# Optimization experiments

Measured on AMD Instinct MI355X. Metric: run time of the kernel, lower is better.

The kernel has to match this reference:

```python
import jax, jax.numpy as jnp
import numpy as np

N_NODES = 20000
N_EDGES = 320000
NODE_DIM = 512
HIDDEN = 512
N_GRAPHS = 64


def setup_inputs() -> dict:
    key = jax.random.key(0)
    ks = jax.random.split(key, 12)
    s = 0.02
    return {
        "joint_x": jax.random.normal(ks[0], (N_NODES, NODE_DIM), jnp.float32),
        "joint_edge_index": jax.random.randint(ks[1], (2, N_EDGES), 0, N_NODES, dtype=jnp.int32),
        "joint_batch": jnp.sort(jax.random.randint(ks[2], (N_NODES,), 0, N_GRAPHS, dtype=jnp.int32)),
        "W_g1": jax.random.normal(ks[3], (NODE_DIM, HIDDEN), jnp.float32) * s,
        "b_g1": jnp.zeros((HIDDEN,), jnp.float32),
        "W_g2": jax.random.normal(ks[4], (HIDDEN, HIDDEN), jnp.float32) * s,
        "b_g2": jnp.zeros((HIDDEN,), jnp.float32),
        "W_c1": jax.random.normal(ks[5], (HIDDEN, HIDDEN // 2), jnp.float32) * s,
        "b_c1": jnp.zeros((HIDDEN // 2,), jnp.float32),
        "W_c2": jax.random.normal(ks[6], (HIDDEN // 2, 1), jnp.float32) * s,
        "b_c2": jnp.zeros((1,), jnp.float32),
    }


def _gin_layer(h, src, dst, W, b):
    # GINConv(nn=Linear, eps=0): nn((1+eps)*x_i + sum_{j->i} x_j)
    agg = jax.ops.segment_sum(h[src], dst, num_segments=N_NODES)  # [N, D]
    return (h + agg) @ W + b


def reference(joint_x, joint_edge_index, joint_batch, W_g1, b_g1, W_g2, b_g2, W_c1, b_c1, W_c2, b_c2):
    src, dst = joint_edge_index[0], joint_edge_index[1]
    h = _gin_layer(joint_x, src, dst, W_g1, b_g1)  # [N, HIDDEN]
    h = _gin_layer(h, src, dst, W_g2, b_g2)        # [N, HIDDEN]
    pooled = jax.ops.segment_sum(h, joint_batch, num_segments=N_GRAPHS)  # [G, HIDDEN]
    z = jax.nn.relu(pooled @ W_c1 + b_c1)
    score = z @ W_c2 + b_c2                        # [G, 1]
    return jax.nn.sigmoid(score).squeeze(-1)       # [G]
```

## Files before the change

### kernel.cpp

```cpp
#include <hip/hip_runtime.h>
#include <math.h>

constexpr int N_NODES = 20000;
constexpr int DIM = 512;
constexpr int NG = 64;
constexpr int CAP = 64;
constexpr int KCH = 80;
constexpr int NCHUNK = (N_NODES + KCH - 1) / KCH;
constexpr int NSPLIT = 2;
constexpr int RSPLIT = 10;
constexpr int CPS = (NCHUNK + RSPLIT - 1) / RSPLIT;
constexpr int CGS = 32;
constexpr int CSTR = 16;
constexpr int NODE_BLOCKS = (N_NODES + 3) / 4;
constexpr int INIT_BLOCKS = (N_NODES + 255) / 256;
constexpr int GEMM_TILES = 17 * 4;
constexpr int KSPLIT_TILES = GEMM_TILES * 2;
constexpr int PQ_ELEMS = 513 * 256;
constexpr int EPT = 2;
constexpr int EDGE_BLOCKS = (320000 + 256 * EPT - 1) / (256 * EPT);

__device__ __forceinline__ int lower_bound_i(const int* __restrict__ a, int n, int v) {
  int lo = 0, hi = n;
  while (lo < hi) {
    int mid = (lo + hi) >> 1;
    if (a[mid] < v) lo = mid + 1; else hi = mid;
  }
  return lo;
}

__global__ __launch_bounds__(256) void node_init(const int* __restrict__ batch,
                                                 int* __restrict__ cursor,
                                                 float* __restrict__ ng,
                                                 float* __restrict__ cgpad, int n_nodes) {
  int node = blockIdx.x * 256 + threadIdx.x;
  if (node < n_nodes) cursor[(size_t)node * CSTR] = 0;
  if (blockIdx.x == 0 && threadIdx.x < 64) {
    int gg = threadIdx.x;
    int s0 = lower_bound_i(batch, n_nodes, gg);
    int e0 = lower_bound_i(batch, n_nodes, gg + 1);
    ng[gg] = (float)(e0 - s0);
    cgpad[gg * CGS] = 0.f;
  }
}

__device__ void gemm_stack_tile(const float* __restrict__ A0, const float* __restrict__ extra,
                                const float* __restrict__ B, const float* __restrict__ B2,
                                float* __restrict__ C,
                                int N, int K, int R0, int tile, int kbeg, int kend,
                                float* As, float* Bs, int tid) {
  int bm = (tile >> 2) * 32;
  int bn = (tile & 3) * 64;
  int tx = tid & 15;
  int ty = tid >> 4;
  int ar = tid >> 3;
  int ac = (tid & 7) * 2;
  int br = tid >> 4;
  int bc = (tid & 15) * 4;
  float acc[2][4] = {};
  for (int k0 = kbeg; k0 < kend; k0 += 16) {
    int row = bm + ar;
    float2 av = make_float2(0.f, 0.f);
    if (row < R0)       av = *(const float2*)(A0 + (size_t)row * K + k0 + ac);
    else if (row == R0) av = *(const float2*)(extra + k0 + ac);
    As[(ac + 0) * 34 + ar] = av.x;
    As[(ac + 1) * 34 + ar] = av.y;
    size_t boff = (size_t)(k0 + br) * N + bn + bc;
    float4 bv = *(const float4*)(B + boff);
    if (B2) {
      float4 b2 = *(const float4*)(B2 + boff);
      bv.x += b2.x; bv.y += b2.y; bv.z += b2.z; bv.w += b2.w;
    }
    *(float4*)&Bs[br * 68 + bc] = bv;
    __syncthreads();
#pragma unroll
    for (int kk = 0; kk < 16; ++kk) {
      float2 a01 = *(const float2*)&As[kk * 34 + ty * 2];
      float4 b4  = *(const float4*)&Bs[kk * 68 + tx * 4];
      acc[0][0] = fmaf(a01.x, b4.x, acc[0][0]); acc[0][1] = fmaf(a01.x, b4.y, acc[0][1]);
      acc[0][2] = fmaf(a01.x, b4.z, acc[0][2]); acc[0][3] = fmaf(a01.x, b4.w, acc[0][3]);
      acc[1][0] = fmaf(a01.y, b4.x, acc[1][0]); acc[1][1] = fmaf(a01.y, b4.y, acc[1][1]);
      acc[1][2] = fmaf(a01.y, b4.z, acc[1][2]); acc[1][3] = fmaf(a01.y, b4.w, acc[1][3]);
    }
    __syncthreads();
  }
#pragma unroll
  for (int i = 0; i < 2; ++i) {
    int m = bm + ty * 2 + i;
    if (m > R0) continue;
    *(float4*)&C[(size_t)m * N + bn + tx * 4] =
        make_float4(acc[i][0], acc[i][1], acc[i][2], acc[i][3]);
  }
}

__global__ __launch_bounds__(256) void fill_and_Q(const int* __restrict__ srcI,
                                                  const int* __restrict__ dstI,
                                                  const int* __restrict__ batch,
                                                  int* __restrict__ cursor,
                                                  int* __restrict__ edst,
                                                  float* __restrict__ cgpad,
                                                  const float* __restrict__ Wg2,
                                                  const float* __restrict__ bg2,
                                                  const float* __restrict__ Wc1,
                                                  float* __restrict__ Q, int n_edges) {
  __shared__ float As[16 * 34];
  __shared__ float Bs[16 * 68];
  __shared__ int hist[64];
  int b = blockIdx.x;
  int t = threadIdx.x;
  if (b < KSPLIT_TILES) {
    int ks = b & 1;
    int tile = b >> 1;
    gemm_stack_tile(Wg2, bg2, Wc1, nullptr, Q + (size_t)ks * PQ_ELEMS,
                    256, 512, 512, tile, ks * 256, ks * 256 + 256, As, Bs, t);
  } else {
    int eb = b - KSPLIT_TILES;
    if (t < 64) hist[t] = 0;
    __syncthreads();
    int base = eb * (256 * EPT) + t;
    int s[EPT], d[EPT], c[EPT];
    bool v[EPT];
#pragma unroll
    for (int u = 0; u < EPT; ++u) {
      int i = base + u * 256;
      v[u] = i < n_edges;
      s[u] = v[u] ? srcI[i] : 0;
    }
#pragma unroll
    for (int u = 0; u < EPT; ++u) {
      int i = base + u * 256;
      d[u] = v[u] ? dstI[i] : 0;
    }
#pragma unroll
    for (int u = 0; u < EPT; ++u)
      if (v[u]) c[u] = atomicAdd(&cursor[(size_t)s[u] * CSTR], 1);
#pragma unroll
    for (int u = 0; u < EPT; ++u)
      if (v[u]) edst[(size_t)s[u] * CAP + c[u]] = d[u];
#pragma unroll
    for (int u = 0; u < EPT; ++u)
      if (v[u]) atomicAdd(&hist[batch[d[u]]], 1);
    __syncthreads();
    if (t < 64 && hist[t] != 0) atomicAdd(&cgpad[t * CGS], (float)hist[t]);
  }
}

__global__ __launch_bounds__(256) void wT_and_P(const int* __restrict__ batch,
                                                const int* __restrict__ deg,
                                                const int* __restrict__ edst,
                                                float* __restrict__ wT,
                                                const float* __restrict__ Wg1,
                                                const float* __restrict__ bg1,
                                                const float* __restrict__ Q,
                                                float* __restrict__ P, int n_nodes) {
  __shared__ float As[16 * 34];
  __shared__ float Bs[16 * 68];
  int b = blockIdx.x;
  int t = threadIdx.x;
  if (b < KSPLIT_TILES) {
    int ks = b & 1;
    int tile = b >> 1;
    gemm_stack_tile(Wg1, bg1, Q, Q + PQ_ELEMS, P + (size_t)ks * PQ_ELEMS,
                    256, 512, 512, tile, ks * 256, ks * 256 + 256, As, Bs, t);
  } else {
    int node = (b - KSPLIT_TILES) * 4 + (t >> 6);
    int g = t & 63;
    if (node >= n_nodes) return;
    int end = deg[(size_t)node * CSTR];
    const int* nb = edst + (size_t)node * CAP;
    float acc = (batch[node] == g) ? 1.f : 0.f;
    int i = 0;
    for (; i + 7 < end; i += 8) {
      int d0 = nb[i], d1 = nb[i + 1], d2 = nb[i + 2], d3 = nb[i + 3];
      int d4 = nb[i + 4], d5 = nb[i + 5], d6 = nb[i + 6], d7 = nb[i + 7];
      int b0 = batch[d0], b1 = batch[d1], b2 = batch[d2], b3 = batch[d3];
      int b4 = batch[d4], b5 = batch[d5], b6 = batch[d6], b7 = batch[d7];
      acc += ((float)(b0 == g) + (float)(b1 == g)) + ((float)(b2 == g) + (float)(b3 == g)) +
             ((float)(b4 == g) + (float)(b5 == g)) + ((float)(b6 == g) + (float)(b7 == g));
    }
    for (; i < end; ++i) acc += (float)(batch[nb[i]] == g);
    wT[(size_t)node * 64 + g] = acc;
  }
}

#define LOADX(X, KB)                                                      \
  _Pragma("unroll")                                                       \
  for (int t_ = 0; t_ < 4; ++t_) {                                        \
    X[t_][0] = x2[(size_t)(k0 + (KB) + t_) * 256 + ncol];                 \
    X[t_][1] = x2[(size_t)(k0 + (KB) + t_) * 256 + ncol + 64];            \
  }

#define COMPX(X, KB)                                                      \
  _Pragma("unroll")                                                       \
  for (int t_ = 0; t_ < 4; ++t_) {                                        \
    const float4* cp_ = (const float4*)&scT[(KB) + t_][w * 8];            \
    float4 cA_ = cp_[0], cB_ = cp_[1];                                    \
    float cv_[8] = {cA_.x, cA_.y, cA_.z, cA_.w, cB_.x, cB_.y, cB_.z, cB_.w}; \
    _Pragma("unroll")                                                     \
    for (int q_ = 0; q_ < 8; ++q_) {                                      \
      acc[q_][0].x = fmaf(cv_[q_], X[t_][0].x, acc[q_][0].x);             \
      acc[q_][0].y = fmaf(cv_[q_], X[t_][0].y, acc[q_][0].y);             \
      acc[q_][1].x = fmaf(cv_[q_], X[t_][1].x, acc[q_][1].x);             \
      acc[q_][1].y = fmaf(cv_[q_], X[t_][1].y, acc[q_][1].y);             \
    }                                                                     \
  }

__global__ __launch_bounds__(512, 4) void ct_ugemm(const float* __restrict__ wT,
                                                   const int* __restrict__ deg,
                                                   const int* __restrict__ edst,
                                                   const float* __restrict__ x,
                                                   float* __restrict__ Upart, int n_nodes) {
  __shared__ float scT[KCH][64];
  int c = blockIdx.y;
  int nx = blockIdx.x;
  int t = threadIdx.x;
  int w = t >> 6;
  int g = t & 63;
  int k0 = c * KCH;
  int kmax = (n_nodes - k0) < KCH ? (n_nodes - k0) : KCH;
  for (int i = w; i < kmax; i += 8) {
    int node = k0 + i;
    float acc1 = wT[(size_t)node * 64 + g];
    int end = deg[(size_t)node * CSTR];
    const int* nb = edst + (size_t)node * CAP;
    int j = 0;
    for (; j + 7 < end; j += 8) {
      int d0 = nb[j], d1 = nb[j + 1], d2 = nb[j + 2], d3 = nb[j + 3];
      int d4 = nb[j + 4], d5 = nb[j + 5], d6 = nb[j + 6], d7 = nb[j + 7];
      float v0 = wT[(size_t)d0 * 64 + g], v1 = wT[(size_t)d1 * 64 + g];
      float v2 = wT[(size_t)d2 * 64 + g], v3 = wT[(size_t)d3 * 64 + g];
      float v4 = wT[(size_t)d4 * 64 + g], v5 = wT[(size_t)d5 * 64 + g];
      float v6 = wT[(size_t)d6 * 64 + g], v7 = wT[(size_t)d7 * 64 + g];
      acc1 += ((v0 + v1) + (v2 + v3)) + ((v4 + v5) + (v6 + v7));
    }
    for (; j + 3 < end; j += 4) {
      int d0 = nb[j], d1 = nb[j + 1], d2 = nb[j + 2], d3 = nb[j + 3];
      acc1 += wT[(size_t)d0 * 64 + g] + wT[(size_t)d1 * 64 + g] +
              wT[(size_t)d2 * 64 + g] + wT[(size_t)d3 * 64 + g];
    }
    for (; j < end; ++j) acc1 += wT[(size_t)nb[j] * 64 + g];
    scT[i][g] = acc1;
  }
  __syncthreads();
  const float2* x2 = (const float2*)x;
  int ncol = nx * 128 + g;
  float2 acc[8][2];
#pragma unroll
  for (int q = 0; q < 8; ++q) {
    acc[q][0] = make_float2(0.f, 0.f);
    acc[q][1] = make_float2(0.f, 0.f);
  }
  float2 xa[4][2], xb[4][2];
  LOADX(xa, 0);
  for (int kk = 0; kk < kmax; kk += 8) {
    LOADX(xb, kk + 4);
    COMPX(xa, kk);
    if (kk + 8 < kmax) { LOADX(xa, kk + 8); }
    COMPX(xb, kk + 4);
  }
  float2* up = (float2*)Upart;
#pragma unroll
  for (int q = 0; q < 8; ++q) {
    int gg = w * 8 + q;
    up[((size_t)c * 64 + gg) * 256 + ncol] = acc[q][0];
    up[((size_t)c * 64 + gg) * 256 + ncol + 64] = acc[q][1];
  }
}

__global__ __launch_bounds__(128) void reduce_U(const float* __restrict__ Upart,
                                                float* __restrict__ Ured) {
  int g = blockIdx.x;
  int s = blockIdx.y;
  int t = threadIdx.x;
  int c0 = s * CPS;
  int c1 = (c0 + CPS < NCHUNK) ? c0 + CPS : NCHUNK;
  const float4* up = (const float4*)Upart;
  float4 acc = make_float4(0.f, 0.f, 0.f, 0.f);
  for (int c = c0; c < c1; ++c) {
    float4 v = up[((size_t)c * 64 + g) * 128 + t];
    acc.x += v.x; acc.y += v.y; acc.z += v.z; acc.w += v.w;
  }
  ((float4*)Ured)[((size_t)s * 64 + g) * 128 + t] = acc;
}

__global__ __launch_bounds__(256) void head(const float* __restrict__ Ured,
                                            const float* __restrict__ P,
                                            const float* __restrict__ Q,
                                            const float* __restrict__ ng,
                                            const float* __restrict__ cgpad,
                                            const float* __restrict__ bc1,
                                            const float* __restrict__ Wc2,
                                            const float* __restrict__ bc2,
                                            float* __restrict__ out) {
  int g = blockIdx.x;
  int j = threadIdx.x;
  const float* Wc0 = P;
  const float* Wc1p = P + (size_t)PQ_ELEMS;
  const float* v1a = P + (size_t)512 * 256;
  const float* v1b = P + (size_t)PQ_ELEMS + (size_t)512 * 256;
  const float* v2a = Q + (size_t)512 * 256;
  const float* v2b = Q + (size_t)PQ_ELEMS + (size_t)512 * 256;
  __shared__ float p[512];
  float s0 = 0.f, s1 = 0.f;
#pragma unroll
  for (int s = 0; s < RSPLIT; ++s) {
    s0 += Ured[((size_t)s * 64 + g) * DIM + j];
    s1 += Ured[((size_t)s * 64 + g) * DIM + 256 + j];
  }
  p[j] = s0;
  p[j + 256] = s1;
  __syncthreads();
  float cg = ng[g] + cgpad[g * CGS];
  float acc = bc1[j] + cg * (v1a[j] + v1b[j]) + ng[g] * (v2a[j] + v2b[j]);
  for (int k = 0; k < 512; ++k) {
    float w = Wc0[k * 256 + j] + Wc1p[k * 256 + j];
    acc = fmaf(p[k], w, acc);
  }
  float z = fmaxf(acc, 0.f);
  float part = z * Wc2[j];
  for (int off = 32; off > 0; off >>= 1) part += __shfl_down(part, off, 64);
  __shared__ float red[4];
  if ((j & 63) == 0) red[j >> 6] = part;
  __syncthreads();
  if (j == 0) {
    float tot = red[0] + red[1] + red[2] + red[3] + bc2[0];
    out[g] = 1.f / (1.f + expf(-tot));
  }
}

extern "C" void kernel_launch(void* const* d_in, const int* in_sizes, int n_in,
                              void* d_out, int out_size, void* d_ws, size_t ws_size,
                              hipStream_t stream) {
  const float* x    = (const float*)d_in[0];
  const int*   ei   = (const int*)d_in[1];
  const int*   batch= (const int*)d_in[2];
  const float* Wg1  = (const float*)d_in[3];
  const float* bg1  = (const float*)d_in[4];
  const float* Wg2  = (const float*)d_in[5];
  const float* bg2  = (const float*)d_in[6];
  const float* Wc1  = (const float*)d_in[7];
  const float* bc1  = (const float*)d_in[8];
  const float* Wc2  = (const float*)d_in[9];
  const float* bc2  = (const float*)d_in[10];
  float* out = (float*)d_out;

  int n_edges = in_sizes[1] / 2;
  int n_nodes = in_sizes[2];
  const int* srcI = ei;
  const int* dstI = ei + n_edges;

  char* ws = (char*)d_ws;
  size_t off = 0;
  auto alloc = [&](size_t bytes) { char* p = ws + off; off += (bytes + 255) & ~(size_t)255; return p; };
  float* wT    = (float*)alloc((size_t)N_NODES * 64 * sizeof(float));
  float* Upart = (float*)alloc((size_t)NCHUNK * 64 * DIM * sizeof(float));
  float* Ured  = (float*)alloc((size_t)RSPLIT * 64 * DIM * sizeof(float));
  float* Q     = (float*)alloc((size_t)2 * PQ_ELEMS * sizeof(float));
  float* P     = (float*)alloc((size_t)2 * PQ_ELEMS * sizeof(float));
  float* ng    = (float*)alloc(NG * sizeof(float));
  float* cgpad = (float*)alloc(NG * CGS * sizeof(float));
  int* cursor  = (int*)alloc((size_t)N_NODES * CSTR * sizeof(int));
  int* edst    = (int*)alloc((size_t)N_NODES * CAP * sizeof(int));

  node_init<<<INIT_BLOCKS, 256, 0, stream>>>(batch, cursor, ng, cgpad, n_nodes);
  fill_and_Q<<<KSPLIT_TILES + EDGE_BLOCKS, 256, 0, stream>>>(srcI, dstI, batch, cursor, edst,
                                                             cgpad, Wg2, bg2, Wc1, Q, n_edges);
  wT_and_P<<<KSPLIT_TILES + NODE_BLOCKS, 256, 0, stream>>>(batch, cursor, edst, wT,
                                                           Wg1, bg1, Q, P, n_nodes);
  ct_ugemm<<<dim3(NSPLIT, NCHUNK), 512, 0, stream>>>(wT, cursor, edst, x, Upart, n_nodes);
  reduce_U<<<dim3(64, RSPLIT), 128, 0, stream>>>(Upart, Ured);
  head<<<NG, 256, 0, stream>>>(Ured, P, Q, ng, cgpad, bc1, Wc2, bc2, out);
}
```

Measured before the change: 234.7 us.

## Split wT build into own kernel and precompute cT before the GEMM

Result: faster. 223.2 us (-4.9%).

```diff
diff --git a/kernel.cpp b/kernel.cpp
--- a/kernel.cpp
+++ b/kernel.cpp
@@ -145,10 +145,33 @@
   }
 }
 
-__global__ __launch_bounds__(256) void wT_and_P(const int* __restrict__ batch,
+__global__ __launch_bounds__(256) void build_wT(const int* __restrict__ batch,
                                                 const int* __restrict__ deg,
                                                 const int* __restrict__ edst,
-                                                float* __restrict__ wT,
+                                                float* __restrict__ wT, int n_nodes) {
+  int node = blockIdx.x * 4 + (threadIdx.x >> 6);
+  int g = threadIdx.x & 63;
+  if (node >= n_nodes) return;
+  int end = deg[(size_t)node * CSTR];
+  const int* nb = edst + (size_t)node * CAP;
+  float acc = (batch[node] == g) ? 1.f : 0.f;
+  int i = 0;
+  for (; i + 7 < end; i += 8) {
+    int d0 = nb[i], d1 = nb[i + 1], d2 = nb[i + 2], d3 = nb[i + 3];
+    int d4 = nb[i + 4], d5 = nb[i + 5], d6 = nb[i + 6], d7 = nb[i + 7];
+    int b0 = batch[d0], b1 = batch[d1], b2 = batch[d2], b3 = batch[d3];
+    int b4 = batch[d4], b5 = batch[d5], b6 = batch[d6], b7 = batch[d7];
+    acc += ((float)(b0 == g) + (float)(b1 == g)) + ((float)(b2 == g) + (float)(b3 == g)) +
+           ((float)(b4 == g) + (float)(b5 == g)) + ((float)(b6 == g) + (float)(b7 == g));
+  }
+  for (; i < end; ++i) acc += (float)(batch[nb[i]] == g);
+  wT[(size_t)node * 64 + g] = acc;
+}
+
+__global__ __launch_bounds__(256) void cT_and_P(const float* __restrict__ wT,
+                                                const int* __restrict__ deg,
+                                                const int* __restrict__ edst,
+                                                float* __restrict__ cT,
                                                 const float* __restrict__ Wg1,
                                                 const float* __restrict__ bg1,
                                                 const float* __restrict__ Q,
@@ -166,20 +189,26 @@
     int node = (b - KSPLIT_TILES) * 4 + (t >> 6);
     int g = t & 63;
     if (node >= n_nodes) return;
+    float acc = wT[(size_t)node * 64 + g];
     int end = deg[(size_t)node * CSTR];
     const int* nb = edst + (size_t)node * CAP;
-    float acc = (batch[node] == g) ? 1.f : 0.f;
     int i = 0;
     for (; i + 7 < end; i += 8) {
       int d0 = nb[i], d1 = nb[i + 1], d2 = nb[i + 2], d3 = nb[i + 3];
       int d4 = nb[i + 4], d5 = nb[i + 5], d6 = nb[i + 6], d7 = nb[i + 7];
-      int b0 = batch[d0], b1 = batch[d1], b2 = batch[d2], b3 = batch[d3];
-      int b4 = batch[d4], b5 = batch[d5], b6 = batch[d6], b7 = batch[d7];
-      acc += ((float)(b0 == g) + (float)(b1 == g)) + ((float)(b2 == g) + (float)(b3 == g)) +
-             ((float)(b4 == g) + (float)(b5 == g)) + ((float)(b6 == g) + (float)(b7 == g));
-    }
-    for (; i < end; ++i) acc += (float)(batch[nb[i]] == g);
-    wT[(size_t)node * 64 + g] = acc;
+      float v0 = wT[(size_t)d0 * 64 + g], v1 = wT[(size_t)d1 * 64 + g];
+      float v2 = wT[(size_t)d2 * 64 + g], v3 = wT[(size_t)d3 * 64 + g];
+      float v4 = wT[(size_t)d4 * 64 + g], v5 = wT[(size_t)d5 * 64 + g];
+      float v6 = wT[(size_t)d6 * 64 + g], v7 = wT[(size_t)d7 * 64 + g];
+      acc += ((v0 + v1) + (v2 + v3)) + ((v4 + v5) + (v6 + v7));
+    }
+    for (; i + 3 < end; i += 4) {
+      int d0 = nb[i], d1 = nb[i + 1], d2 = nb[i + 2], d3 = nb[i + 3];
+      acc += wT[(size_t)d0 * 64 + g] + wT[(size_t)d1 * 64 + g] +
+             wT[(size_t)d2 * 64 + g] + wT[(size_t)d3 * 64 + g];
+    }
+    for (; i < end; ++i) acc += wT[(size_t)nb[i] * 64 + g];
+    cT[(size_t)node * 64 + g] = acc;
   }
 }
 
@@ -205,11 +234,9 @@
     }                                                                     \
   }
 
-__global__ __launch_bounds__(512, 4) void ct_ugemm(const float* __restrict__ wT,
-                                                   const int* __restrict__ deg,
-                                                   const int* __restrict__ edst,
-                                                   const float* __restrict__ x,
-                                                   float* __restrict__ Upart, int n_nodes) {
+__global__ __launch_bounds__(512, 4) void ugemm(const float* __restrict__ x,
+                                                const float* __restrict__ cT,
+                                                float* __restrict__ Upart, int n_nodes) {
   __shared__ float scT[KCH][64];
   int c = blockIdx.y;
   int nx = blockIdx.x;
@@ -218,28 +245,11 @@
   int g = t & 63;
   int k0 = c * KCH;
   int kmax = (n_nodes - k0) < KCH ? (n_nodes - k0) : KCH;
-  for (int i = w; i < kmax; i += 8) {
-    int node = k0 + i;
-    float acc1 = wT[(size_t)node * 64 + g];
-    int end = deg[(size_t)node * CSTR];
-    const int* nb = edst + (size_t)node * CAP;
-    int j = 0;
-    for (; j + 7 < end; j += 8) {
-      int d0 = nb[j], d1 = nb[j + 1], d2 = nb[j + 2], d3 = nb[j + 3];
-      int d4 = nb[j + 4], d5 = nb[j + 5], d6 = nb[j + 6], d7 = nb[j + 7];
-      float v0 = wT[(size_t)d0 * 64 + g], v1 = wT[(size_t)d1 * 64 + g];
-      float v2 = wT[(size_t)d2 * 64 + g], v3 = wT[(size_t)d3 * 64 + g];
-      float v4 = wT[(size_t)d4 * 64 + g], v5 = wT[(size_t)d5 * 64 + g];
-      float v6 = wT[(size_t)d6 * 64 + g], v7 = wT[(size_t)d7 * 64 + g];
-      acc1 += ((v0 + v1) + (v2 + v3)) + ((v4 + v5) + (v6 + v7));
-    }
-    for (; j + 3 < end; j += 4) {
-      int d0 = nb[j], d1 = nb[j + 1], d2 = nb[j + 2], d3 = nb[j + 3];
-      acc1 += wT[(size_t)d0 * 64 + g] + wT[(size_t)d1 * 64 + g] +
-              wT[(size_t)d2 * 64 + g] + wT[(size_t)d3 * 64 + g];
-    }
-    for (; j < end; ++j) acc1 += wT[(size_t)nb[j] * 64 + g];
-    scT[i][g] = acc1;
+  {
+    const float4* src = (const float4*)(cT + (size_t)k0 * 64);
+    float4* dst = (float4*)(&scT[0][0]);
+    int limit4 = kmax * 16;
+    for (int i = t; i < limit4; i += 512) dst[i] = src[i];
   }
   __syncthreads();
   const float2* x2 = (const float2*)x;
@@ -353,6 +363,7 @@
   size_t off = 0;
   auto alloc = [&](size_t bytes) { char* p = ws + off; off += (bytes + 255) & ~(size_t)255; return p; };
   float* wT    = (float*)alloc((size_t)N_NODES * 64 * sizeof(float));
+  float* cT    = (float*)alloc((size_t)N_NODES * 64 * sizeof(float));
   float* Upart = (float*)alloc((size_t)NCHUNK * 64 * DIM * sizeof(float));
   float* Ured  = (float*)alloc((size_t)RSPLIT * 64 * DIM * sizeof(float));
   float* Q     = (float*)alloc((size_t)2 * PQ_ELEMS * sizeof(float));
@@ -365,9 +376,10 @@
   node_init<<<INIT_BLOCKS, 256, 0, stream>>>(batch, cursor, ng, cgpad, n_nodes);
   fill_and_Q<<<KSPLIT_TILES + EDGE_BLOCKS, 256, 0, stream>>>(srcI, dstI, batch, cursor, edst,
                                                              cgpad, Wg2, bg2, Wc1, Q, n_edges);
-  wT_and_P<<<KSPLIT_TILES + NODE_BLOCKS, 256, 0, stream>>>(batch, cursor, edst, wT,
+  build_wT<<<NODE_BLOCKS, 256, 0, stream>>>(batch, cursor, edst, wT, n_nodes);
+  cT_and_P<<<KSPLIT_TILES + NODE_BLOCKS, 256, 0, stream>>>(wT, cursor, edst, cT,
                                                            Wg1, bg1, Q, P, n_nodes);
-  ct_ugemm<<<dim3(NSPLIT, NCHUNK), 512, 0, stream>>>(wT, cursor, edst, x, Upart, n_nodes);
+  ugemm<<<dim3(NSPLIT, NCHUNK), 512, 0, stream>>>(x, cT, Upart, n_nodes);
   reduce_U<<<dim3(64, RSPLIT), 128, 0, stream>>>(Upart, Ured);
   head<<<NG, 256, 0, stream>>>(Ured, P, Q, ng, cgpad, bc1, Wc2, bc2, out);
 }
```
